# Kernel optimization log

Hardware: AMD Instinct MI355X
Metric: run time of the kernel (lower is better)

## Reference

```python
import jax, jax.numpy as jnp
import numpy as np

POOL = 2

def conv1x1(x, w, b):
    # x: [B,C,H,W], w: [O,C], b: [O]
    return jnp.einsum('bchw,oc->bohw', x, w) + b[None, :, None, None]

def setup_inputs() -> dict:
    key = jax.random.key(0)
    ks = jax.random.split(key, 8)
    B, C, H, W = 4, 256, 128, 128
    C8 = C // 8
    x = jax.random.normal(ks[0], (B, C, H, W), dtype=jnp.float32)
    wq = jax.random.normal(ks[1], (C8, C), dtype=jnp.float32) * 0.05
    bq = jax.random.normal(ks[2], (C8,), dtype=jnp.float32) * 0.01
    wk = jax.random.normal(ks[3], (C8, C), dtype=jnp.float32) * 0.05
    bk = jax.random.normal(ks[4], (C8,), dtype=jnp.float32) * 0.01
    wv = jax.random.normal(ks[5], (C, C), dtype=jnp.float32) * 0.05
    bv = jax.random.normal(ks[6], (C,), dtype=jnp.float32) * 0.01
    gamma = jnp.full((1,), 0.5, dtype=jnp.float32)  # module inits to 0; nonzero for a meaningful baseline
    return {"x": x, "wq": wq, "bq": bq, "wk": wk, "bk": bk, "wv": wv, "bv": bv, "gamma": gamma}

def reference(x, wq, bq, wk, bk, wv, bv, gamma):
    B, C, H, W = x.shape
    y = x
    # AvgPool2d(pool_size=2)
    Hp, Wp = H // POOL, W // POOL
    xp = x.reshape(B, C, Hp, POOL, Wp, POOL).mean(axis=(3, 5))
    N = Hp * Wp
    q = conv1x1(xp, wq, bq).reshape(B, -1, N)            # [B, C/8, N]
    k = conv1x1(xp, wk, bk).reshape(B, -1, N)            # [B, C/8, N]
    v = conv1x1(xp, wv, bv).reshape(B, C, N)             # [B, C, N]
    energy = jnp.einsum('bcn,bcm->bnm', q, k)            # [B, N, N]
    attn = jax.nn.softmax(energy, axis=-1)
    out = jnp.einsum('bcm,bnm->bcn', v, attn)            # [B, C, N]
    out = out.reshape(B, C, Hp, Wp)
    # bilinear upsample x2, align_corners=False == half-pixel == jax.image.resize 'linear'
    up = jax.image.resize(out, (B, C, H, W), method='bilinear')
    return gamma[0] * up + y
```

## Files before the change

kernel.cpp:

```cpp
#include <hip/hip_runtime.h>

#define BB 4
#define CC 256
#define HH 128
#define WW 128
#define HP 64
#define NP 4096

#define L2E 1.4426950408889634f

typedef __attribute__((ext_vector_type(4)))  float f32x4;
typedef __attribute__((ext_vector_type(16))) float f32x16;
typedef __attribute__((ext_vector_type(8)))  short bf16x8;
typedef __attribute__((ext_vector_type(4)))  unsigned int u32x4;
typedef __attribute__((ext_vector_type(2)))  unsigned int u32x2;
typedef __attribute__((ext_vector_type(2)))  __bf16 bf16x2_t;

static __device__ __forceinline__ float exp2fast(float x) {
    return __builtin_amdgcn_exp2f(x);
}

static __device__ __forceinline__ unsigned short f2bf(float f) {
    unsigned int u = __float_as_uint(f);
    u = (u + 0x7FFFu + ((u >> 16) & 1u)) >> 16;
    return (unsigned short)u;
}
static __device__ __forceinline__ unsigned int pk2(float a, float b) {
    bf16x2_t v = {(__bf16)a, (__bf16)b};
    return __builtin_bit_cast(unsigned int, v);
}
static __device__ __forceinline__ u32x2 plswap(unsigned int a, unsigned int b) {
    return __builtin_amdgcn_permlane32_swap(a, b, false, false);
}


__global__ __launch_bounds__(256) void prep_kernel(const float* __restrict__ x,
                                                   const float* __restrict__ wq,
                                                   const float* __restrict__ wk,
                                                   const float* __restrict__ wv,
                                                   unsigned short* __restrict__ xfrag,
                                                   unsigned short* __restrict__ wfrag) {
    if (blockIdx.x < 2048) {
        int tid  = blockIdx.x * 256 + threadIdx.x;
        int lane = tid & 63;
        int ks   = (tid >> 6) & 15;
        int nt   = (tid >> 10) & 127;
        int b    = tid >> 17;

        int n  = nt * 32 + (lane & 31);
        int c0 = ks * 16 + (lane >> 5) * 8;
        int hp = n >> 6, wp = n & 63;

        const float* xb = x + (size_t)b * CC * (HH * WW) + (2 * hp) * WW + 2 * wp;
        unsigned short r[8];
        #pragma unroll
        for (int e = 0; e < 8; e++) {
            const float* src = xb + (size_t)(c0 + e) * (HH * WW);
            float2 a = *(const float2*)(src);
            float2 d = *(const float2*)(src + WW);
            r[e] = f2bf(0.25f * (a.x + a.y + d.x + d.y));
        }
        ushort4 lo = (ushort4){r[0], r[1], r[2], r[3]};
        ushort4 hi = (ushort4){r[4], r[5], r[6], r[7]};
        *(ushort4*)(xfrag + (size_t)tid * 8)     = lo;
        *(ushort4*)(xfrag + (size_t)tid * 8 + 4) = hi;
    } else {
        int tid  = (blockIdx.x - 2048) * 256 + threadIdx.x;
        if (tid >= 10240) return;
        int lane = tid & 63;
        int ks   = (tid >> 6) & 15;
        int ot   = tid >> 10;

        int o = ot * 32 + (lane & 31);
        int c = ks * 16 + (lane >> 5) * 8;
        const float* wrow;
        float scale = 1.0f;
        if (o < 32)      { wrow = wq + (size_t)o * CC;        scale = L2E; }
        else if (o < 64) { wrow = wk + (size_t)(o - 32) * CC; }
        else             { wrow = wv + (size_t)(o - 64) * CC; }
        float4 w0 = *(const float4*)(wrow + c);
        float4 w1 = *(const float4*)(wrow + c + 4);
        ushort4 lo = {f2bf(w0.x * scale), f2bf(w0.y * scale), f2bf(w0.z * scale), f2bf(w0.w * scale)};
        ushort4 hi = {f2bf(w1.x * scale), f2bf(w1.y * scale), f2bf(w1.z * scale), f2bf(w1.w * scale)};
        *(ushort4*)(wfrag + (size_t)tid * 8)     = lo;
        *(ushort4*)(wfrag + (size_t)tid * 8 + 4) = hi;
    }
}

__global__ __launch_bounds__(128) void projm_kernel(const unsigned short* __restrict__ xfrag,
                                                    const unsigned short* __restrict__ wfrag,
                                                    const float* __restrict__ bq,
                                                    const float* __restrict__ bk,
                                                    const float* __restrict__ bv,
                                                    unsigned short* __restrict__ qarr,
                                                    unsigned short* __restrict__ karr,
                                                    unsigned short* __restrict__ varr) {
    int j    = blockIdx.x;
    int og   = j % 5;
    int nt   = (j / 5) & 127;
    int b    = j / 640;
    int lane = threadIdx.x & 63;
    int ot   = og * 2 + (threadIdx.x >> 6);

    const unsigned short* abase = wfrag + ((size_t)ot * 16 * 64 + lane) * 8;
    const unsigned short* bbase = xfrag + (((size_t)(b * 128 + nt) * 16) * 64 + lane) * 8;

    f32x16 acc;
    #pragma unroll
    for (int r = 0; r < 16; r++) acc[r] = 0.f;

    #pragma unroll
    for (int ks = 0; ks < 16; ks++) {
        bf16x8 af = *(const bf16x8*)(abase + (size_t)ks * 512);
        bf16x8 bf = *(const bf16x8*)(bbase + (size_t)ks * 512);
        acc = __builtin_amdgcn_mfma_f32_32x32x16_bf16(af, bf, acc, 0, 0, 0);
    }

    int l31 = lane & 31;
    int hi2 = lane >> 5;

    if (ot == 0) {
        unsigned short* qb = qarr + (size_t)b * (NP * 32);
        #pragma unroll
        for (int r = 0; r < 16; r++) {
            int o = (r & 3) + 8 * (r >> 2) + 4 * hi2;
            float v = acc[r] + bq[o] * L2E;
            size_t idx = (((size_t)nt * 2 + (o >> 4)) * 32 + l31) * 16 + ((o >> 3) & 1) * 8 + (o & 7);
            qb[idx] = f2bf(v);
        }
    } else if (ot == 1) {
        unsigned short* kb = karr + (size_t)b * (NP * 32);
        #pragma unroll
        for (int r = 0; r < 16; r++) {
            int o = (r & 3) + 8 * (r >> 2) + 4 * hi2;
            float v = acc[r] + bk[o];
            size_t idx = (((size_t)nt * 2 + (o >> 4)) * 32 + l31) * 16 + ((o >> 3) & 1) * 8 + (o & 7);
            kb[idx] = f2bf(v);
        }
    } else {
        unsigned short* vb = varr + (size_t)b * (CC * NP);
        int kc = nt, w2 = (l31 >> 4) & 1, hiv = (l31 >> 3) & 1, ev = l31 & 7;
        size_t base = (((size_t)kc * 2 + w2) * 8) * 32 * 16 + hiv * 8 + ev;
        #pragma unroll
        for (int r = 0; r < 16; r++) {
            int c = (ot - 2) * 32 + (r & 3) + 8 * (r >> 2) + 4 * hi2;
            float v = acc[r] + bv[c];
            size_t idx = base + ((size_t)(c >> 5) * 32 + (c & 31)) * 16;
            vb[idx] = f2bf(v);
        }
    }
}

__global__ __launch_bounds__(512, 2) void flash32_kernel(const unsigned short* __restrict__ qarr,
                                                         const unsigned short* __restrict__ karr,
                                                         const unsigned short* __restrict__ varr,
                                                         float* __restrict__ att) {
    __shared__ float cacc[2][64][68];
    __shared__ float cml[2][64][2];
    int t    = threadIdx.x;
    int lane = t & 63;
    int w    = t >> 6;
    int ch   = w & 1;
    int ks   = w >> 1;
    int j    = blockIdx.x;
    int b    = j & 3;
    int st   = j >> 2;
    int qt0  = st * 2, qt1 = qt0 + 1;

    const unsigned short* qb2 = qarr + (size_t)b * (NP * 32);
    const unsigned short* kb2 = karr + (size_t)b * (NP * 32);
    const unsigned short* vb2 = varr + (size_t)b * (CC * NP);

    int q  = lane & 31;
    int hi = lane >> 5;
    int lq16 = (q * 2 + hi) * 8;

    bf16x8 qA0 = *(const bf16x8*)(qb2 + (size_t)(qt0 * 2 + 0) * 512 + lq16);
    bf16x8 qA1 = *(const bf16x8*)(qb2 + (size_t)(qt0 * 2 + 1) * 512 + lq16);
    bf16x8 qB0 = *(const bf16x8*)(qb2 + (size_t)(qt1 * 2 + 0) * 512 + lq16);
    bf16x8 qB1 = *(const bf16x8*)(qb2 + (size_t)(qt1 * 2 + 1) * 512 + lq16);

    f32x16 accA[4], accB[4];
    #pragma unroll
    for (int ct = 0; ct < 4; ct++)
        #pragma unroll
        for (int r = 0; r < 16; r++) { accA[ct][r] = 0.f; accB[ct][r] = 0.f; }
    float mrunA = -3.0e38f, lrunA = 0.f;
    float mrunB = -3.0e38f, lrunB = 0.f;

    const f32x16 z16 = {0.f,0.f,0.f,0.f,0.f,0.f,0.f,0.f,0.f,0.f,0.f,0.f,0.f,0.f,0.f,0.f};

    int kc0 = ks * 32;
    const unsigned short* kcp0 = kb2 + (size_t)kc0 * 1024 + lq16;
    bf16x8 kcur0 = *(const bf16x8*)(kcp0);
    bf16x8 kcur1 = *(const bf16x8*)(kcp0 + 512);

    for (int kci = 0; kci < 32; ++kci) {
        int kcidx = kc0 + kci;
        int nid = (kci < 31) ? (kcidx + 1) : kcidx;

        const unsigned short* vcp = vb2 + ((size_t)kcidx * 16 + ch * 4) * 512 + lq16;
        bf16x8 vf[8];
        #pragma unroll
        for (int w2 = 0; w2 < 2; w2++)
            #pragma unroll
            for (int i = 0; i < 4; i++)
                vf[w2 * 4 + i] = *(const bf16x8*)(vcp + (size_t)(w2 * 8 + i) * 512);

        const unsigned short* kn = kb2 + (size_t)nid * 1024 + lq16;
        bf16x8 kn0 = *(const bf16x8*)(kn);
        bf16x8 kn1 = *(const bf16x8*)(kn + 512);

        f32x16 sA = __builtin_amdgcn_mfma_f32_32x32x16_bf16(kcur0, qA0, z16, 0, 0, 0);
        sA = __builtin_amdgcn_mfma_f32_32x32x16_bf16(kcur1, qA1, sA, 0, 0, 0);
        f32x16 sB = __builtin_amdgcn_mfma_f32_32x32x16_bf16(kcur0, qB0, z16, 0, 0, 0);
        sB = __builtin_amdgcn_mfma_f32_32x32x16_bf16(kcur1, qB1, sB, 0, 0, 0);

        unsigned int pkrA[8];
        {
            float m01 = fmaxf(sA[0], sA[1]),   m23 = fmaxf(sA[2], sA[3]);
            float m45 = fmaxf(sA[4], sA[5]),   m67 = fmaxf(sA[6], sA[7]);
            float m89 = fmaxf(sA[8], sA[9]),   mab = fmaxf(sA[10], sA[11]);
            float mcd = fmaxf(sA[12], sA[13]), mef = fmaxf(sA[14], sA[15]);
            float mx = fmaxf(fmaxf(fmaxf(m01, m23), fmaxf(m45, m67)),
                             fmaxf(fmaxf(m89, mab), fmaxf(mcd, mef)));
            u32x2 mr = plswap(__float_as_uint(mx), __float_as_uint(mx));
            mx = fmaxf(__uint_as_float(mr.x), __uint_as_float(mr.y));
            if (!__all(mx - mrunA <= 11.5f)) {
                float mn = fmaxf(mrunA, mx);
                float sc = exp2fast(mrunA - mn);
                mrunA = mn;
                lrunA *= sc;
                #pragma unroll
                for (int ct = 0; ct < 4; ct++)
                    #pragma unroll
                    for (int r = 0; r < 16; r++) accA[ct][r] *= sc;
            }
            float ps[8];
            #pragma unroll
            for (int r2 = 0; r2 < 8; r2++) {
                float p0 = exp2fast(sA[2 * r2]     - mrunA);
                float p1 = exp2fast(sA[2 * r2 + 1] - mrunA);
                ps[r2] = p0 + p1;
                pkrA[r2] = pk2(p0, p1);
            }
            float s01 = ps[0] + ps[1], s23 = ps[2] + ps[3];
            float s45 = ps[4] + ps[5], s67 = ps[6] + ps[7];
            float ssum = (s01 + s23) + (s45 + s67);
            u32x2 sr = plswap(__float_as_uint(ssum), __float_as_uint(ssum));
            lrunA += __uint_as_float(sr.x) + __uint_as_float(sr.y);
        }

        unsigned int pkrB[8];
        {
            float m01 = fmaxf(sB[0], sB[1]),   m23 = fmaxf(sB[2], sB[3]);
            float m45 = fmaxf(sB[4], sB[5]),   m67 = fmaxf(sB[6], sB[7]);
            float m89 = fmaxf(sB[8], sB[9]),   mab = fmaxf(sB[10], sB[11]);
            float mcd = fmaxf(sB[12], sB[13]), mef = fmaxf(sB[14], sB[15]);
            float mx = fmaxf(fmaxf(fmaxf(m01, m23), fmaxf(m45, m67)),
                             fmaxf(fmaxf(m89, mab), fmaxf(mcd, mef)));
            u32x2 mr = plswap(__float_as_uint(mx), __float_as_uint(mx));
            mx = fmaxf(__uint_as_float(mr.x), __uint_as_float(mr.y));
            if (!__all(mx - mrunB <= 11.5f)) {
                float mn = fmaxf(mrunB, mx);
                float sc = exp2fast(mrunB - mn);
                mrunB = mn;
                lrunB *= sc;
                #pragma unroll
                for (int ct = 0; ct < 4; ct++)
                    #pragma unroll
                    for (int r = 0; r < 16; r++) accB[ct][r] *= sc;
            }
            float ps[8];
            #pragma unroll
            for (int r2 = 0; r2 < 8; r2++) {
                float p0 = exp2fast(sB[2 * r2]     - mrunB);
                float p1 = exp2fast(sB[2 * r2 + 1] - mrunB);
                ps[r2] = p0 + p1;
                pkrB[r2] = pk2(p0, p1);
            }
            float s01 = ps[0] + ps[1], s23 = ps[2] + ps[3];
            float s45 = ps[4] + ps[5], s67 = ps[6] + ps[7];
            float ssum = (s01 + s23) + (s45 + s67);
            u32x2 sr = plswap(__float_as_uint(ssum), __float_as_uint(ssum));
            lrunB += __uint_as_float(sr.x) + __uint_as_float(sr.y);
        }

        #pragma unroll
        for (int w2 = 0; w2 < 2; w2++) {
            u32x2 rA0 = plswap(pkrA[4 * w2 + 0], pkrA[4 * w2 + 2]);
            u32x2 rA1 = plswap(pkrA[4 * w2 + 1], pkrA[4 * w2 + 3]);
            u32x4 frA; frA[0] = rA0.x; frA[1] = rA1.x; frA[2] = rA0.y; frA[3] = rA1.y;
            bf16x8 pfA = __builtin_bit_cast(bf16x8, frA);
            u32x2 rB0 = plswap(pkrB[4 * w2 + 0], pkrB[4 * w2 + 2]);
            u32x2 rB1 = plswap(pkrB[4 * w2 + 1], pkrB[4 * w2 + 3]);
            u32x4 frB; frB[0] = rB0.x; frB[1] = rB1.x; frB[2] = rB0.y; frB[3] = rB1.y;
            bf16x8 pfB = __builtin_bit_cast(bf16x8, frB);
            #pragma unroll
            for (int ct = 0; ct < 4; ct++) {
                accA[ct] = __builtin_amdgcn_mfma_f32_32x32x16_bf16(vf[w2 * 4 + ct], pfA, accA[ct], 0, 0, 0);
                accB[ct] = __builtin_amdgcn_mfma_f32_32x32x16_bf16(vf[w2 * 4 + ct], pfB, accB[ct], 0, 0, 0);
            }
        }

        kcur0 = kn0; kcur1 = kn1;
    }

    #pragma unroll
    for (int tile = 0; tile < 2; tile++) {
        for (int sIdx = 3; sIdx >= 1; --sIdx) {
            if (ks == sIdx) {
                #pragma unroll
                for (int ct = 0; ct < 4; ct++)
                    #pragma unroll
                    for (int rr = 0; rr < 4; rr++) {
                        float4 v4;
                        if (tile == 0)
                            v4 = (float4){accA[ct][rr*4+0], accA[ct][rr*4+1], accA[ct][rr*4+2], accA[ct][rr*4+3]};
                        else
                            v4 = (float4){accB[ct][rr*4+0], accB[ct][rr*4+1], accB[ct][rr*4+2], accB[ct][rr*4+3]};
                        *(float4*)&cacc[ch][lane][ct * 16 + rr * 4] = v4;
                    }
                cml[ch][lane][0] = (tile == 0) ? mrunA : mrunB;
                cml[ch][lane][1] = (tile == 0) ? lrunA : lrunB;
            }
            __syncthreads();
            if (ks == 0) {
                float mo = cml[ch][lane][0];
                float lo = cml[ch][lane][1];
                float mr = (tile == 0) ? mrunA : mrunB;
                float mn = fmaxf(mr, mo);
                float e0 = exp2fast(mr - mn);
                float e1 = exp2fast(mo - mn);
                if (tile == 0) { mrunA = mn; lrunA = lrunA * e0 + lo * e1; }
                else           { mrunB = mn; lrunB = lrunB * e0 + lo * e1; }
                #pragma unroll
                for (int ct = 0; ct < 4; ct++)
                    #pragma unroll
                    for (int r = 0; r < 16; r++) {
                        if (tile == 0)
                            accA[ct][r] = accA[ct][r] * e0 + cacc[ch][lane][ct * 16 + r] * e1;
                        else
                            accB[ct][r] = accB[ct][r] * e0 + cacc[ch][lane][ct * 16 + r] * e1;
                    }
            }
            __syncthreads();
        }
    }

    if (ks == 0) {
        float invA = 1.0f / lrunA;
        float invB = 1.0f / lrunB;
        #pragma unroll
        for (int ct = 0; ct < 4; ct++)
            #pragma unroll
            for (int r = 0; r < 16; r++) {
                int c = ch * 128 + ct * 32 + (r & 3) + 8 * (r >> 2) + 4 * hi;
                float* ob = att + ((size_t)b * CC + c) * NP;
                ob[qt0 * 32 + q] = accA[ct][r] * invA;
                ob[qt1 * 32 + q] = accB[ct][r] * invB;
            }
    }
}

__global__ __launch_bounds__(256) void upsample_kernel(const float* __restrict__ att,
                                                       const float* __restrict__ x,
                                                       const float* __restrict__ gamma,
                                                       float* __restrict__ out) {
    int tid = blockIdx.x * 256 + threadIdx.x;
    int w4 = (tid & 31) * 4;
    int h  = (tid >> 5) & 127;
    int bc = tid >> 12;
    float g = gamma[0];

    float sh = 0.5f * h - 0.25f;
    float fhf = floorf(sh);
    float th = sh - fhf;
    int ih = (int)fhf;
    int ih0 = ih < 0 ? 0 : ih;
    int ih1 = ih + 1 > 63 ? 63 : ih + 1;
    const float* a0r = att + (size_t)bc * NP + ih0 * 64;
    const float* a1r = att + (size_t)bc * NP + ih1 * 64;

    float4 xin = *(const float4*)(x + (size_t)bc * (HH * WW) + h * WW + w4);
    float xv[4] = {xin.x, xin.y, xin.z, xin.w};
    float ov[4];
    #pragma unroll
    for (int k = 0; k < 4; k++) {
        int w = w4 + k;
        float sw = 0.5f * w - 0.25f;
        float fwf = floorf(sw);
        float tw = sw - fwf;
        int iw = (int)fwf;
        int iw0 = iw < 0 ? 0 : iw;
        int iw1 = iw + 1 > 63 ? 63 : iw + 1;
        float v00 = a0r[iw0], v01 = a0r[iw1];
        float v10 = a1r[iw0], v11 = a1r[iw1];
        float top = v00 + tw * (v01 - v00);
        float bot = v10 + tw * (v11 - v10);
        float up  = top + th * (bot - top);
        ov[k] = g * up + xv[k];
    }
    float4 o4 = {ov[0], ov[1], ov[2], ov[3]};
    *(float4*)(out + (size_t)bc * (HH * WW) + h * WW + w4) = o4;
}

extern "C" void kernel_launch(void* const* d_in, const int* in_sizes, int n_in,
                              void* d_out, int out_size, void* d_ws, size_t ws_size,
                              hipStream_t stream) {
    (void)in_sizes; (void)n_in; (void)out_size; (void)ws_size;
    const float* x     = (const float*)d_in[0];
    const float* wq    = (const float*)d_in[1];
    const float* bq    = (const float*)d_in[2];
    const float* wk    = (const float*)d_in[3];
    const float* bk    = (const float*)d_in[4];
    const float* wv    = (const float*)d_in[5];
    const float* bv    = (const float*)d_in[6];
    const float* gamma = (const float*)d_in[7];
    float* out = (float*)d_out;

    unsigned short* xfrag = (unsigned short*)d_ws;
    unsigned short* wfrag = xfrag + 4194304;
    unsigned short* qarr  = wfrag + 131072;
    unsigned short* karr  = qarr + 524288;
    unsigned short* varr  = karr + 524288;
    float*          att   = (float*)(varr + 4194304);

    prep_kernel<<<2088, 256, 0, stream>>>(x, wq, wk, wv, xfrag, wfrag);
    projm_kernel<<<2560, 128, 0, stream>>>(xfrag, wfrag, bq, bk, bv, qarr, karr, varr);
    flash32_kernel<<<256, 512, 0, stream>>>(qarr, karr, varr, att);
    upsample_kernel<<<16384, 256, 0, stream>>>(att, x, gamma, out);
}
```

Baseline: 119.2 us.

## Split softmax work between channel-half waves and exchange probabilities via LDS

Each wave pair previously computed QK^T scores and softmax for both query tiles redundantly. Now each wave computes scores and softmax for only its own query tile and exchanges the packed probabilities and rescale factor with its partner wave through shared memory each iteration. This halves the score MFMAs and exp work. In exchange it adds a block-wide barrier per key chunk. The cross-split merge is also restructured: max/sum statistics are reduced once up front, so the final accumulation becomes plain adds.

```diff
diff --git a/kernel.cpp b/kernel.cpp
--- a/kernel.cpp
+++ b/kernel.cpp
@@ -155,8 +155,9 @@
                                                          const unsigned short* __restrict__ karr,
                                                          const unsigned short* __restrict__ varr,
                                                          float* __restrict__ att) {
+    __shared__ float exch[2][4][2][64][9];
     __shared__ float cacc[2][64][68];
-    __shared__ float cml[2][64][2];
+    __shared__ float cmlT[2][4][64][2];
     int t    = threadIdx.x;
     int lane = t & 63;
     int w    = t >> 6;
@@ -166,6 +167,7 @@
     int b    = j & 3;
     int st   = j >> 2;
     int qt0  = st * 2, qt1 = qt0 + 1;
+    int qtOwn = qt0 + ch;
 
     const unsigned short* qb2 = qarr + (size_t)b * (NP * 32);
     const unsigned short* kb2 = karr + (size_t)b * (NP * 32);
@@ -175,18 +177,15 @@
     int hi = lane >> 5;
     int lq16 = (q * 2 + hi) * 8;
 
-    bf16x8 qA0 = *(const bf16x8*)(qb2 + (size_t)(qt0 * 2 + 0) * 512 + lq16);
-    bf16x8 qA1 = *(const bf16x8*)(qb2 + (size_t)(qt0 * 2 + 1) * 512 + lq16);
-    bf16x8 qB0 = *(const bf16x8*)(qb2 + (size_t)(qt1 * 2 + 0) * 512 + lq16);
-    bf16x8 qB1 = *(const bf16x8*)(qb2 + (size_t)(qt1 * 2 + 1) * 512 + lq16);
+    bf16x8 qf0 = *(const bf16x8*)(qb2 + (size_t)(qtOwn * 2 + 0) * 512 + lq16);
+    bf16x8 qf1 = *(const bf16x8*)(qb2 + (size_t)(qtOwn * 2 + 1) * 512 + lq16);
 
     f32x16 accA[4], accB[4];
     #pragma unroll
     for (int ct = 0; ct < 4; ct++)
         #pragma unroll
         for (int r = 0; r < 16; r++) { accA[ct][r] = 0.f; accB[ct][r] = 0.f; }
-    float mrunA = -3.0e38f, lrunA = 0.f;
-    float mrunB = -3.0e38f, lrunB = 0.f;
+    float mrun = -3.0e38f, lrun = 0.f;
 
     const f32x16 z16 = {0.f,0.f,0.f,0.f,0.f,0.f,0.f,0.f,0.f,0.f,0.f,0.f,0.f,0.f,0.f,0.f};
 
@@ -198,6 +197,7 @@
     for (int kci = 0; kci < 32; ++kci) {
         int kcidx = kc0 + kci;
         int nid = (kci < 31) ? (kcidx + 1) : kcidx;
+        int p = kci & 1;
 
         const unsigned short* vcp = vb2 + ((size_t)kcidx * 16 + ch * 4) * 512 + lq16;
         bf16x8 vf[8];
@@ -211,79 +211,80 @@
         bf16x8 kn0 = *(const bf16x8*)(kn);
         bf16x8 kn1 = *(const bf16x8*)(kn + 512);
 
-        f32x16 sA = __builtin_amdgcn_mfma_f32_32x32x16_bf16(kcur0, qA0, z16, 0, 0, 0);
-        sA = __builtin_amdgcn_mfma_f32_32x32x16_bf16(kcur1, qA1, sA, 0, 0, 0);
-        f32x16 sB = __builtin_amdgcn_mfma_f32_32x32x16_bf16(kcur0, qB0, z16, 0, 0, 0);
-        sB = __builtin_amdgcn_mfma_f32_32x32x16_bf16(kcur1, qB1, sB, 0, 0, 0);
-
-        unsigned int pkrA[8];
+        f32x16 s = __builtin_amdgcn_mfma_f32_32x32x16_bf16(kcur0, qf0, z16, 0, 0, 0);
+        s = __builtin_amdgcn_mfma_f32_32x32x16_bf16(kcur1, qf1, s, 0, 0, 0);
+
+        unsigned int pkr[8];
+        float sc = 1.0f;
         {
-            float m01 = fmaxf(sA[0], sA[1]),   m23 = fmaxf(sA[2], sA[3]);
-            float m45 = fmaxf(sA[4], sA[5]),   m67 = fmaxf(sA[6], sA[7]);
-            float m89 = fmaxf(sA[8], sA[9]),   mab = fmaxf(sA[10], sA[11]);
-            float mcd = fmaxf(sA[12], sA[13]), mef = fmaxf(sA[14], sA[15]);
+            float m01 = fmaxf(s[0], s[1]),   m23 = fmaxf(s[2], s[3]);
+            float m45 = fmaxf(s[4], s[5]),   m67 = fmaxf(s[6], s[7]);
+            float m89 = fmaxf(s[8], s[9]),   mab = fmaxf(s[10], s[11]);
+            float mcd = fmaxf(s[12], s[13]), mef = fmaxf(s[14], s[15]);
             float mx = fmaxf(fmaxf(fmaxf(m01, m23), fmaxf(m45, m67)),
                              fmaxf(fmaxf(m89, mab), fmaxf(mcd, mef)));
             u32x2 mr = plswap(__float_as_uint(mx), __float_as_uint(mx));
             mx = fmaxf(__uint_as_float(mr.x), __uint_as_float(mr.y));
-            if (!__all(mx - mrunA <= 11.5f)) {
-                float mn = fmaxf(mrunA, mx);
-                float sc = exp2fast(mrunA - mn);
-                mrunA = mn;
-                lrunA *= sc;
-                #pragma unroll
-                for (int ct = 0; ct < 4; ct++)
-                    #pragma unroll
-                    for (int r = 0; r < 16; r++) accA[ct][r] *= sc;
+            if (!__all(mx - mrun <= 11.5f)) {
+                float mn = fmaxf(mrun, mx);
+                sc = exp2fast(mrun - mn);
+                mrun = mn;
+                lrun *= sc;
             }
             float ps[8];
             #pragma unroll
             for (int r2 = 0; r2 < 8; r2++) {
-                float p0 = exp2fast(sA[2 * r2]     - mrunA);
-                float p1 = exp2fast(sA[2 * r2 + 1] - mrunA);
+                float p0 = exp2fast(s[2 * r2]     - mrun);
+                float p1 = exp2fast(s[2 * r2 + 1] - mrun);
                 ps[r2] = p0 + p1;
-                pkrA[r2] = pk2(p0, p1);
+                pkr[r2] = pk2(p0, p1);
             }
             float s01 = ps[0] + ps[1], s23 = ps[2] + ps[3];
             float s45 = ps[4] + ps[5], s67 = ps[6] + ps[7];
             float ssum = (s01 + s23) + (s45 + s67);
             u32x2 sr = plswap(__float_as_uint(ssum), __float_as_uint(ssum));
-            lrunA += __uint_as_float(sr.x) + __uint_as_float(sr.y);
-        }
-
-        unsigned int pkrB[8];
+            lrun += __uint_as_float(sr.x) + __uint_as_float(sr.y);
+        }
+
         {
-            float m01 = fmaxf(sB[0], sB[1]),   m23 = fmaxf(sB[2], sB[3]);
-            float m45 = fmaxf(sB[4], sB[5]),   m67 = fmaxf(sB[6], sB[7]);
-            float m89 = fmaxf(sB[8], sB[9]),   mab = fmaxf(sB[10], sB[11]);
-            float mcd = fmaxf(sB[12], sB[13]), mef = fmaxf(sB[14], sB[15]);
-            float mx = fmaxf(fmaxf(fmaxf(m01, m23), fmaxf(m45, m67)),
-                             fmaxf(fmaxf(m89, mab), fmaxf(mcd, mef)));
-            u32x2 mr = plswap(__float_as_uint(mx), __float_as_uint(mx));
-            mx = fmaxf(__uint_as_float(mr.x), __uint_as_float(mr.y));
-            if (!__all(mx - mrunB <= 11.5f)) {
-                float mn = fmaxf(mrunB, mx);
-                float sc = exp2fast(mrunB - mn);
-                mrunB = mn;
-                lrunB *= sc;
+            float* slot = exch[p][ks][ch][lane];
+            #pragma unroll
+            for (int i = 0; i < 8; i++) slot[i] = __uint_as_float(pkr[i]);
+            slot[8] = sc;
+        }
+        __syncthreads();
+        unsigned int pkrO[8];
+        float scO;
+        {
+            const float* oth = exch[p][ks][ch ^ 1][lane];
+            #pragma unroll
+            for (int i = 0; i < 8; i++) pkrO[i] = __float_as_uint(oth[i]);
+            scO = oth[8];
+        }
+
+        unsigned int pkrA[8], pkrB[8];
+        float scA, scB;
+        if (ch == 0) {
+            #pragma unroll
+            for (int i = 0; i < 8; i++) { pkrA[i] = pkr[i]; pkrB[i] = pkrO[i]; }
+            scA = sc; scB = scO;
+        } else {
+            #pragma unroll
+            for (int i = 0; i < 8; i++) { pkrA[i] = pkrO[i]; pkrB[i] = pkr[i]; }
+            scA = scO; scB = sc;
+        }
+
+        if (!__all(scA == 1.0f)) {
+            #pragma unroll
+            for (int ct = 0; ct < 4; ct++)
                 #pragma unroll
-                for (int ct = 0; ct < 4; ct++)
-                    #pragma unroll
-                    for (int r = 0; r < 16; r++) accB[ct][r] *= sc;
-            }
-            float ps[8];
-            #pragma unroll
-            for (int r2 = 0; r2 < 8; r2++) {
-                float p0 = exp2fast(sB[2 * r2]     - mrunB);
-                float p1 = exp2fast(sB[2 * r2 + 1] - mrunB);
-                ps[r2] = p0 + p1;
-                pkrB[r2] = pk2(p0, p1);
-            }
-            float s01 = ps[0] + ps[1], s23 = ps[2] + ps[3];
-            float s45 = ps[4] + ps[5], s67 = ps[6] + ps[7];
-            float ssum = (s01 + s23) + (s45 + s67);
-            u32x2 sr = plswap(__float_as_uint(ssum), __float_as_uint(ssum));
-            lrunB += __uint_as_float(sr.x) + __uint_as_float(sr.y);
+                for (int r = 0; r < 16; r++) accA[ct][r] *= scA;
+        }
+        if (!__all(scB == 1.0f)) {
+            #pragma unroll
+            for (int ct = 0; ct < 4; ct++)
+                #pragma unroll
+                for (int r = 0; r < 16; r++) accB[ct][r] *= scB;
         }
 
         #pragma unroll
@@ -305,6 +306,31 @@
 
         kcur0 = kn0; kcur1 = kn1;
     }
+
+    cmlT[ch][ks][lane][0] = mrun;
+    cmlT[ch][ks][lane][1] = lrun;
+    __syncthreads();
+    float eA[4], eB[4], invA, invB;
+    {
+        float mA = fmaxf(fmaxf(cmlT[0][0][lane][0], cmlT[0][1][lane][0]),
+                         fmaxf(cmlT[0][2][lane][0], cmlT[0][3][lane][0]));
+        float mB = fmaxf(fmaxf(cmlT[1][0][lane][0], cmlT[1][1][lane][0]),
+                         fmaxf(cmlT[1][2][lane][0], cmlT[1][3][lane][0]));
+        float lA = 0.f, lB = 0.f;
+        #pragma unroll
+        for (int sI = 0; sI < 4; sI++) {
+            eA[sI] = exp2fast(cmlT[0][sI][lane][0] - mA);
+            eB[sI] = exp2fast(cmlT[1][sI][lane][0] - mB);
+            lA += cmlT[0][sI][lane][1] * eA[sI];
+            lB += cmlT[1][sI][lane][1] * eB[sI];
+        }
+        invA = 1.0f / lA;
+        invB = 1.0f / lB;
+    }
+    #pragma unroll
+    for (int ct = 0; ct < 4; ct++)
+        #pragma unroll
+        for (int r = 0; r < 16; r++) { accA[ct][r] *= eA[ks]; accB[ct][r] *= eB[ks]; }
 
     #pragma unroll
     for (int tile = 0; tile < 2; tile++) {
@@ -321,27 +347,15 @@
                             v4 = (float4){accB[ct][rr*4+0], accB[ct][rr*4+1], accB[ct][rr*4+2], accB[ct][rr*4+3]};
                         *(float4*)&cacc[ch][lane][ct * 16 + rr * 4] = v4;
                     }
-                cml[ch][lane][0] = (tile == 0) ? mrunA : mrunB;
-                cml[ch][lane][1] = (tile == 0) ? lrunA : lrunB;
             }
             __syncthreads();
             if (ks == 0) {
-                float mo = cml[ch][lane][0];
-                float lo = cml[ch][lane][1];
-                float mr = (tile == 0) ? mrunA : mrunB;
-                float mn = fmaxf(mr, mo);
-                float e0 = exp2fast(mr - mn);
-                float e1 = exp2fast(mo - mn);
-                if (tile == 0) { mrunA = mn; lrunA = lrunA * e0 + lo * e1; }
-                else           { mrunB = mn; lrunB = lrunB * e0 + lo * e1; }
                 #pragma unroll
                 for (int ct = 0; ct < 4; ct++)
                     #pragma unroll
                     for (int r = 0; r < 16; r++) {
-                        if (tile == 0)
-                            accA[ct][r] = accA[ct][r] * e0 + cacc[ch][lane][ct * 16 + r] * e1;
-                        else
-                            accB[ct][r] = accB[ct][r] * e0 + cacc[ch][lane][ct * 16 + r] * e1;
+                        if (tile == 0) accA[ct][r] += cacc[ch][lane][ct * 16 + r];
+                        else           accB[ct][r] += cacc[ch][lane][ct * 16 + r];
                     }
             }
             __syncthreads();
@@ -349,8 +363,6 @@
     }
 
     if (ks == 0) {
-        float invA = 1.0f / lrunA;
-        float invB = 1.0f / lrunB;
         #pragma unroll
         for (int ct = 0; ct < 4; ct++)
             #pragma unroll
```

Result: faster. 114.9 us (-3.6%).
